# Optimization experiments

Hardware: AMD Instinct MI355X
Metric: run time of the kernel (lower is better)

Reference implementation:

```python
import jax, jax.numpy as jnp
import numpy as np

NFEAT, NHID = 128, 128

def setup_inputs() -> dict:
    key = jax.random.key(0)
    k1, k2, k3, k4 = jax.random.split(key, 4)
    x = jax.random.normal(k1, (32, 1024, NFEAT), dtype=jnp.float32)
    adj = jax.random.uniform(k2, (32, 1024, 1024), dtype=jnp.float32)
    # GraphConvolution parameters (Kipf init ~ uniform, scale irrelevant for correctness)
    bound = 1.0 / np.sqrt(NHID)
    W = jax.random.uniform(k3, (NFEAT, NHID), dtype=jnp.float32, minval=-bound, maxval=bound)
    b = jax.random.uniform(k4, (NHID,), dtype=jnp.float32, minval=-bound, maxval=bound)
    return {"x": x, "adj": adj, "W": W, "b": b}

def reference(x, adj, W, b):
    # Batched equivalent of the per-sample python loop:
    # out[i] = relu(adj[i] @ (x[i] @ W) + b); dropout is identity in eval mode.
    support = jnp.einsum('bnf,fh->bnh', x, W)          # [B, N, nhid]
    out = jnp.einsum('bnm,bmh->bnh', adj, support) + b  # [B, N, nhid]
    return jax.nn.relu(out)
```

## Files before the change

kernel.cpp:

```cpp
#include <hip/hip_runtime.h>
#include <stdint.h>


typedef short bf16x8 __attribute__((ext_vector_type(8)));
typedef float f32x4 __attribute__((ext_vector_type(4)));
typedef int i32x4 __attribute__((ext_vector_type(4)));
typedef unsigned short u16x4 __attribute__((ext_vector_type(4)));

__device__ __forceinline__ unsigned short f2bf(float f) {
    uint32_t u = __builtin_bit_cast(uint32_t, f);
    u += 0x7FFFu + ((u >> 16) & 1u);
    return (unsigned short)(u >> 16);
}

__global__ __launch_bounds__(256) void k0_wt(const float* __restrict__ W,
                                             unsigned short* __restrict__ WT) {
    int o = blockIdx.x * 256 + threadIdx.x;
    int h = o >> 7, f = o & 127;
    WT[o] = f2bf(W[f * 128 + h]);
}

#define K1S 136
__global__ __launch_bounds__(256) void k1_support(const float* __restrict__ x,
                                                  const unsigned short* __restrict__ WT,
                                                  unsigned short* __restrict__ ST) {
    __shared__ __align__(16) unsigned short xt[64 * K1S];
    __shared__ __align__(16) unsigned short wt[128 * K1S];
    int t = threadIdx.x;
    int node_base = blockIdx.x * 64;

    const f32x4* xg = (const f32x4*)(x + (size_t)node_base * 128);
#pragma unroll
    for (int i = 0; i < 8; ++i) {
        int f4 = i * 256 + t;
        int row = f4 >> 5, c4 = f4 & 31;
        f32x4 v = xg[f4];
        u16x4 p;
        p.x = f2bf(v.x); p.y = f2bf(v.y); p.z = f2bf(v.z); p.w = f2bf(v.w);
        *(u16x4*)&xt[row * K1S + c4 * 4] = p;
    }
    const i32x4* wg = (const i32x4*)WT;
#pragma unroll
    for (int i = 0; i < 8; ++i) {
        int c = i * 256 + t;
        int row = c >> 4, ch = c & 15;
        *(i32x4*)&wt[row * K1S + ch * 8] = wg[c];
    }
    __syncthreads();

    int wv = t >> 6, lane = t & 63, l16 = lane & 15, quad = lane >> 4;
    int wave_h = (wv & 1) * 64, wave_m = (wv >> 1) * 32;

    f32x4 acc[4][2];
#pragma unroll
    for (int ht = 0; ht < 4; ++ht)
#pragma unroll
        for (int mt = 0; mt < 2; ++mt) acc[ht][mt] = 0.f;

#pragma unroll
    for (int s = 0; s < 4; ++s) {
        int ko = s * 32 + quad * 8;
        bf16x8 a[4], bb[2];
#pragma unroll
        for (int ht = 0; ht < 4; ++ht)
            a[ht] = *(const bf16x8*)&wt[(wave_h + ht * 16 + l16) * K1S + ko];
#pragma unroll
        for (int mt = 0; mt < 2; ++mt)
            bb[mt] = *(const bf16x8*)&xt[(wave_m + mt * 16 + l16) * K1S + ko];
#pragma unroll
        for (int ht = 0; ht < 4; ++ht)
#pragma unroll
            for (int mt = 0; mt < 2; ++mt)
                acc[ht][mt] = __builtin_amdgcn_mfma_f32_16x16x32_bf16(
                    a[ht], bb[mt], acc[ht][mt], 0, 0, 0);
    }

    int batch = blockIdx.x >> 4;
    int m_in_b = (blockIdx.x & 15) * 64;
#pragma unroll
    for (int ht = 0; ht < 4; ++ht)
#pragma unroll
        for (int mt = 0; mt < 2; ++mt) {
            int mcol = wave_m + mt * 16 + l16;
#pragma unroll
            for (int r = 0; r < 4; ++r) {
                int h = wave_h + ht * 16 + quad * 4 + r;
                ST[(((size_t)batch * 128 + h) << 10) + m_in_b + mcol] =
                    f2bf(acc[ht][mt][r]);
            }
        }
}

#define K2S 72
__global__ __launch_bounds__(256) void k2_gcn(const float* __restrict__ adj,
                                              const unsigned short* __restrict__ ST,
                                              const float* __restrict__ bias,
                                              float* __restrict__ out) {
    __shared__ __align__(16) unsigned short As[64 * K2S];
    __shared__ __align__(16) unsigned short Bs[128 * K2S];
    int t = threadIdx.x;
    int batch = blockIdx.x >> 4;
    int mbase = (blockIdx.x & 15) * 64;
    int wv = t >> 6, lane = t & 63, l16 = lane & 15, quad = lane >> 4;
    int wave_m = (wv & 1) * 32, wave_n = (wv >> 1) * 64;

    float bv[4];
#pragma unroll
    for (int j = 0; j < 4; ++j) bv[j] = bias[wave_n + j * 16 + l16];

    f32x4 acc[2][4];
#pragma unroll
    for (int i = 0; i < 2; ++i)
#pragma unroll
        for (int j = 0; j < 4; ++j) acc[i][j] = 0.f;

    const float* adjb = adj + ((size_t)batch * 1024 + mbase) * 1024;
    const unsigned short* stb = ST + ((size_t)batch * 128) * 1024;

    for (int kb = 0; kb < 16; ++kb) {
#pragma unroll
        for (int i = 0; i < 4; ++i) {
            int f4 = i * 256 + t;
            int row = f4 >> 4, c4 = f4 & 15;
            f32x4 v = *(const f32x4*)(adjb + (size_t)row * 1024 + kb * 64 + c4 * 4);
            u16x4 p;
            p.x = f2bf(v.x); p.y = f2bf(v.y); p.z = f2bf(v.z); p.w = f2bf(v.w);
            *(u16x4*)&As[row * K2S + c4 * 4] = p;
        }
#pragma unroll
        for (int i = 0; i < 4; ++i) {
            int c = i * 256 + t;
            int row = c >> 3, ch = c & 7;
            *(i32x4*)&Bs[row * K2S + ch * 8] =
                *(const i32x4*)(stb + (size_t)row * 1024 + kb * 64 + ch * 8);
        }
        __syncthreads();
#pragma unroll
        for (int s = 0; s < 2; ++s) {
            int ko = s * 32 + quad * 8;
            bf16x8 a[2], bb[4];
#pragma unroll
            for (int i = 0; i < 2; ++i)
                a[i] = *(const bf16x8*)&As[(wave_m + i * 16 + l16) * K2S + ko];
#pragma unroll
            for (int j = 0; j < 4; ++j)
                bb[j] = *(const bf16x8*)&Bs[(wave_n + j * 16 + l16) * K2S + ko];
#pragma unroll
            for (int i = 0; i < 2; ++i)
#pragma unroll
                for (int j = 0; j < 4; ++j)
                    acc[i][j] = __builtin_amdgcn_mfma_f32_16x16x32_bf16(
                        a[i], bb[j], acc[i][j], 0, 0, 0);
        }
        __syncthreads();
    }

    float* outb = out + ((size_t)batch * 1024 + mbase) * 128;
#pragma unroll
    for (int i = 0; i < 2; ++i)
#pragma unroll
        for (int j = 0; j < 4; ++j) {
            int n = wave_n + j * 16 + l16;
#pragma unroll
            for (int r = 0; r < 4; ++r) {
                int m = wave_m + i * 16 + quad * 4 + r;
                float v = acc[i][j][r] + bv[j];
                outb[(size_t)m * 128 + n] = fmaxf(v, 0.f);
            }
        }
}

extern "C" void kernel_launch(void* const* d_in, const int* in_sizes, int n_in,
                              void* d_out, int out_size, void* d_ws, size_t ws_size,
                              hipStream_t stream) {
    const float* x = (const float*)d_in[0];
    const float* adj = (const float*)d_in[1];
    const float* W = (const float*)d_in[2];
    const float* b = (const float*)d_in[3];
    float* out = (float*)d_out;

    unsigned short* ST = (unsigned short*)d_ws;
    unsigned short* WT = (unsigned short*)d_ws + (size_t)32 * 128 * 1024;

    k0_wt<<<64, 256, 0, stream>>>(W, WT);
    k1_support<<<512, 256, 0, stream>>>(x, WT, ST);
    k2_gcn<<<512, 256, 0, stream>>>(adj, ST, b, out);
}
```

Before: 225.5 us.

## Load adj and support tiles directly to LDS with swizzle; fold W transpose into k1

The GCN kernel now stages fp32 adj tiles and bf16 support tiles with global_load_lds DMA into XOR-swizzled LDS layouts, and converts adj to bf16 only when reading MFMA operands. This drops the register round-trip and the separate conversion and store pass during staging. The W transpose/convert kernel is removed, and each k1 block instead transposes W into LDS itself, which saves one launch but makes every block repeat that work with scalar LDS writes. fp32 adj in LDS doubles the A-tile footprint, and the loop still runs single-buffered with two barriers per iteration.

Measured after the change: 229.7 us. Within noise of the previous version (+1.9%).

```diff
diff --git a/kernel.cpp b/kernel.cpp
--- a/kernel.cpp
+++ b/kernel.cpp
@@ -1,4 +1,5 @@
 #include <hip/hip_runtime.h>
+#include <hip/hip_bf16.h>
 #include <stdint.h>
 
 
@@ -13,16 +14,23 @@
     return (unsigned short)(u >> 16);
 }
 
-__global__ __launch_bounds__(256) void k0_wt(const float* __restrict__ W,
-                                             unsigned short* __restrict__ WT) {
-    int o = blockIdx.x * 256 + threadIdx.x;
-    int h = o >> 7, f = o & 127;
-    WT[o] = f2bf(W[f * 128 + h]);
-}
+__device__ __forceinline__ bf16x8 cvt8(f32x4 v0, f32x4 v1) {
+    union { __hip_bfloat162 h[4]; bf16x8 v; } u;
+    u.h[0] = __float22bfloat162_rn(make_float2(v0.x, v0.y));
+    u.h[1] = __float22bfloat162_rn(make_float2(v0.z, v0.w));
+    u.h[2] = __float22bfloat162_rn(make_float2(v1.x, v1.y));
+    u.h[3] = __float22bfloat162_rn(make_float2(v1.z, v1.w));
+    return u.v;
+}
+
+#define GLOAD_LDS16(g, s)                                         \
+    __builtin_amdgcn_global_load_lds(                             \
+        (const __attribute__((address_space(1))) void*)(g),       \
+        (__attribute__((address_space(3))) void*)(s), 16, 0, 0)
 
 #define K1S 136
 __global__ __launch_bounds__(256) void k1_support(const float* __restrict__ x,
-                                                  const unsigned short* __restrict__ WT,
+                                                  const float* __restrict__ W,
                                                   unsigned short* __restrict__ ST) {
     __shared__ __align__(16) unsigned short xt[64 * K1S];
     __shared__ __align__(16) unsigned short wt[128 * K1S];
@@ -39,12 +47,15 @@
         p.x = f2bf(v.x); p.y = f2bf(v.y); p.z = f2bf(v.z); p.w = f2bf(v.w);
         *(u16x4*)&xt[row * K1S + c4 * 4] = p;
     }
-    const i32x4* wg = (const i32x4*)WT;
-#pragma unroll
-    for (int i = 0; i < 8; ++i) {
+#pragma unroll
+    for (int i = 0; i < 16; ++i) {
         int c = i * 256 + t;
-        int row = c >> 4, ch = c & 15;
-        *(i32x4*)&wt[row * K1S + ch * 8] = wg[c];
+        int f = c >> 5, h4 = c & 31;
+        f32x4 v = *(const f32x4*)(W + f * 128 + h4 * 4);
+        wt[(h4 * 4 + 0) * K1S + f] = f2bf(v.x);
+        wt[(h4 * 4 + 1) * K1S + f] = f2bf(v.y);
+        wt[(h4 * 4 + 2) * K1S + f] = f2bf(v.z);
+        wt[(h4 * 4 + 3) * K1S + f] = f2bf(v.w);
     }
     __syncthreads();
 
@@ -91,60 +102,70 @@
         }
 }
 
-#define K2S 72
 __global__ __launch_bounds__(256) void k2_gcn(const float* __restrict__ adj,
                                               const unsigned short* __restrict__ ST,
                                               const float* __restrict__ bias,
                                               float* __restrict__ out) {
-    __shared__ __align__(16) unsigned short As[64 * K2S];
-    __shared__ __align__(16) unsigned short Bs[128 * K2S];
-    int t = threadIdx.x;
-    int batch = blockIdx.x >> 4;
-    int mbase = (blockIdx.x & 15) * 64;
-    int wv = t >> 6, lane = t & 63, l16 = lane & 15, quad = lane >> 4;
-    int wave_m = (wv & 1) * 32, wave_n = (wv >> 1) * 64;
-
-    float bv[4];
-#pragma unroll
-    for (int j = 0; j < 4; ++j) bv[j] = bias[wave_n + j * 16 + l16];
-
-    f32x4 acc[2][4];
-#pragma unroll
-    for (int i = 0; i < 2; ++i)
-#pragma unroll
-        for (int j = 0; j < 4; ++j) acc[i][j] = 0.f;
+    __shared__ __align__(16) float As[64 * 64];
+    __shared__ __align__(16) unsigned short Bs[128 * 64];
+    const int t = threadIdx.x;
+    const int wv = t >> 6, l = t & 63, l16 = l & 15, quad = l >> 4;
+    const int batch = blockIdx.x >> 4;
+    const int mbase = (blockIdx.x & 15) * 64;
 
     const float* adjb = adj + ((size_t)batch * 1024 + mbase) * 1024;
     const unsigned short* stb = ST + ((size_t)batch * 128) * 1024;
 
+    const int cA = l & 15, cB = l & 7;
+    const float* gA[4];
+    const unsigned short* gB[4];
+    float* ldsA[4];
+    unsigned short* ldsB[4];
+#pragma unroll
+    for (int i = 0; i < 4; ++i) {
+        int ra = wv * 16 + i * 4 + (l >> 4);
+        gA[i] = adjb + (size_t)ra * 1024 + ((cA ^ (2 * (ra & 7))) << 2);
+        ldsA[i] = &As[(wv * 16 + i * 4) * 64];
+        int rb = wv * 32 + i * 8 + (l >> 3);
+        gB[i] = stb + (size_t)rb * 1024 + ((cB ^ (rb & 7)) << 3);
+        ldsB[i] = &Bs[(wv * 32 + i * 8) * 64];
+    }
+
+    const int wave_m = (wv & 1) * 32, wave_n = (wv >> 1) * 64;
+    float bv[4];
+#pragma unroll
+    for (int j = 0; j < 4; ++j) bv[j] = bias[wave_n + j * 16 + l16];
+
+    f32x4 acc[2][4];
+#pragma unroll
+    for (int i = 0; i < 2; ++i)
+#pragma unroll
+        for (int j = 0; j < 4; ++j) acc[i][j] = 0.f;
+
     for (int kb = 0; kb < 16; ++kb) {
 #pragma unroll
         for (int i = 0; i < 4; ++i) {
-            int f4 = i * 256 + t;
-            int row = f4 >> 4, c4 = f4 & 15;
-            f32x4 v = *(const f32x4*)(adjb + (size_t)row * 1024 + kb * 64 + c4 * 4);
-            u16x4 p;
-            p.x = f2bf(v.x); p.y = f2bf(v.y); p.z = f2bf(v.z); p.w = f2bf(v.w);
-            *(u16x4*)&As[row * K2S + c4 * 4] = p;
-        }
-#pragma unroll
-        for (int i = 0; i < 4; ++i) {
-            int c = i * 256 + t;
-            int row = c >> 3, ch = c & 7;
-            *(i32x4*)&Bs[row * K2S + ch * 8] =
-                *(const i32x4*)(stb + (size_t)row * 1024 + kb * 64 + ch * 8);
+            GLOAD_LDS16(gA[i] + kb * 64, ldsA[i]);
+            GLOAD_LDS16(gB[i] + kb * 64, ldsB[i]);
         }
         __syncthreads();
 #pragma unroll
         for (int s = 0; s < 2; ++s) {
-            int ko = s * 32 + quad * 8;
             bf16x8 a[2], bb[4];
 #pragma unroll
-            for (int i = 0; i < 2; ++i)
-                a[i] = *(const bf16x8*)&As[(wave_m + i * 16 + l16) * K2S + ko];
-#pragma unroll
-            for (int j = 0; j < 4; ++j)
-                bb[j] = *(const bf16x8*)&Bs[(wave_n + j * 16 + l16) * K2S + ko];
+            for (int i = 0; i < 2; ++i) {
+                int ra = wave_m + i * 16 + l16;
+                int pp = (((s * 4 + quad) ^ (ra & 7)) << 3);
+                f32x4 v0 = *(const f32x4*)&As[ra * 64 + pp];
+                f32x4 v1 = *(const f32x4*)&As[ra * 64 + pp + 4];
+                a[i] = cvt8(v0, v1);
+            }
+#pragma unroll
+            for (int j = 0; j < 4; ++j) {
+                int nb = wave_n + j * 16 + l16;
+                int cc = (((s * 4 + quad) ^ (nb & 7)) << 3);
+                bb[j] = *(const bf16x8*)&Bs[nb * 64 + cc];
+            }
 #pragma unroll
             for (int i = 0; i < 2; ++i)
 #pragma unroll
@@ -180,9 +201,7 @@
     float* out = (float*)d_out;
 
     unsigned short* ST = (unsigned short*)d_ws;
-    unsigned short* WT = (unsigned short*)d_ws + (size_t)32 * 128 * 1024;
-
-    k0_wt<<<64, 256, 0, stream>>>(W, WT);
-    k1_support<<<512, 256, 0, stream>>>(x, WT, ST);
+
+    k1_support<<<512, 256, 0, stream>>>(x, W, ST);
     k2_gcn<<<512, 256, 0, stream>>>(adj, ST, b, out);
 }
```
